# Kernel tuning notes

Hardware: AMD Instinct MI355X
Metric: run time of the kernel (lower is better)

Reference implementation:

```python
import jax, jax.numpy as jnp
import numpy as np

N_NODES = 50000
N_EDGES = 1250000
VOCAB = 50000
EMBED = 64
HIDDEN = 64
NUM_REL = 3
N_CLASSES = 2
N_GRAPHS = 512


def setup_inputs() -> dict:
    key = jax.random.key(0)
    ks = jax.random.split(key, 12)
    x = jax.random.randint(ks[0], (N_NODES,), 0, VOCAB, dtype=jnp.int32)
    edge_index = jax.random.randint(ks[1], (2, N_EDGES), 0, N_NODES, dtype=jnp.int32)
    edge_type = jax.random.randint(ks[2], (N_EDGES,), 0, NUM_REL, dtype=jnp.int32)
    batch = jnp.sort(jax.random.randint(ks[3], (N_NODES,), 0, N_GRAPHS, dtype=jnp.int32))
    s = 0.05
    emb = jax.random.normal(ks[4], (VOCAB, EMBED), jnp.float32) * s
    w1_rel = jax.random.normal(ks[5], (NUM_REL, EMBED, HIDDEN), jnp.float32) * s
    w1_root = jax.random.normal(ks[6], (EMBED, HIDDEN), jnp.float32) * s
    b1 = jnp.zeros((HIDDEN,), jnp.float32)
    w2_rel = jax.random.normal(ks[7], (NUM_REL, HIDDEN, HIDDEN), jnp.float32) * s
    w2_root = jax.random.normal(ks[8], (HIDDEN, HIDDEN), jnp.float32) * s
    b2 = jnp.zeros((HIDDEN,), jnp.float32)
    lin_w = jax.random.normal(ks[9], (HIDDEN, N_CLASSES), jnp.float32) * s
    lin_b = jnp.zeros((N_CLASSES,), jnp.float32)
    return {"x": x, "edge_index": edge_index, "edge_type": edge_type, "batch": batch,
            "emb": emb, "w1_rel": w1_rel, "w1_root": w1_root, "b1": b1,
            "w2_rel": w2_rel, "w2_root": w2_root, "b2": b2,
            "lin_w": lin_w, "lin_b": lin_b}


def rgcn_conv(h, src, dst, edge_type, w_rel, w_root, bias):
    # PyG RGCNConv: out = h @ W_root + bias + sum_r mean-aggregated (h_src @ W_r)
    out = h @ w_root + bias
    h_src = h[src]  # [E, F] gather
    for r in range(NUM_REL):
        mask = (edge_type == r).astype(h.dtype)  # [E]
        m = (h_src @ w_rel[r]) * mask[:, None]   # [E, H]
        s = jax.ops.segment_sum(m, dst, num_segments=N_NODES)
        cnt = jax.ops.segment_sum(mask, dst, num_segments=N_NODES)
        out = out + s / jnp.maximum(cnt, 1.0)[:, None]
    return out


def reference(x, edge_index, edge_type, batch, emb, w1_rel, w1_root, b1,
              w2_rel, w2_root, b2, lin_w, lin_b):
    src, dst = edge_index[0], edge_index[1]
    emb_eff = emb.at[0].set(0.0)  # padding_idx=0
    h = emb_eff[x]  # [N, EMBED]
    h = jax.nn.relu(rgcn_conv(h, src, dst, edge_type, w1_rel, w1_root, b1))
    h = jax.nn.relu(rgcn_conv(h, src, dst, edge_type, w2_rel, w2_root, b2))
    # global mean pool over graphs
    sums = jax.ops.segment_sum(h, batch, num_segments=N_GRAPHS)
    cnt = jax.ops.segment_sum(jnp.ones((h.shape[0],), h.dtype), batch, num_segments=N_GRAPHS)
    pooled = sums / jnp.maximum(cnt, 1.0)[:, None]  # [G, HIDDEN]
    return pooled @ lin_w + lin_b  # [G, N_CLASSES]
```

## Files before the change

### kernel.cpp

```cpp
#include <hip/hip_runtime.h>

#define CHUNK 2048

__global__ __launch_bounds__(256) void embed_count_kernel(
    const int* __restrict__ x, const float* __restrict__ emb, float* __restrict__ h0,
    const int* __restrict__ ei, int* __restrict__ pcount,
    int n_nodes, int n_edges, int n_bkt, int embed_blocks)
{
    __shared__ int cnt[512];
    int t = threadIdx.x;
    if ((int)blockIdx.x < embed_blocks) {
        int tt = blockIdx.x * 256 + t;
        if (tt < n_nodes * 16) {
            int n = tt >> 4, q = tt & 15;
            int xv = x[n];
            float4 v = {0.f, 0.f, 0.f, 0.f};
            if (xv != 0) v = *(const float4*)(emb + (size_t)xv * 64 + q * 4);
            *(float4*)(h0 + (size_t)n * 64 + q * 4) = v;
        }
        return;
    }
    int jb = blockIdx.x - embed_blocks;
    for (int b = t; b < 512; b += 256) cnt[b] = 0;
    __syncthreads();
    int base = jb * CHUNK;
#pragma unroll
    for (int i = 0; i < CHUNK / 256; ++i) {
        int e = base + i * 256 + t;
        if (e < n_edges) atomicAdd(&cnt[ei[n_edges + e] >> 7], 1);
    }
    __syncthreads();
    for (int b = t; b < n_bkt; b += 256) pcount[jb * n_bkt + b] = cnt[b];
}

__global__ __launch_bounds__(256) void colscan_kernel(
    const int* __restrict__ pcount, int* __restrict__ pre,
    int* __restrict__ totals, int* __restrict__ rowstartR,
    int n_chk, int n_bkt, int n_edges, int n_nodes)
{
    __shared__ int ps[256];
    int b = blockIdx.x, t = threadIdx.x;
    if (b == 0 && t == 0) rowstartR[4 * n_nodes] = n_edges;
    int v[4], s = 0;
#pragma unroll
    for (int i = 0; i < 4; ++i) {
        int jj = t * 4 + i;
        v[i] = (jj < n_chk) ? pcount[jj * n_bkt + b] : 0;
        s += v[i];
    }
    ps[t] = s;
    __syncthreads();
    for (int o = 1; o < 256; o <<= 1) {
        int u = (t >= o) ? ps[t - o] : 0;
        __syncthreads();
        ps[t] += u;
        __syncthreads();
    }
    int run = (t > 0) ? ps[t - 1] : 0;
#pragma unroll
    for (int i = 0; i < 4; ++i) {
        int jj = t * 4 + i;
        if (jj < n_chk) pre[jj * n_bkt + b] = run;
        run += v[i];
    }
    if (t == 255) totals[b] = run;
}

__global__ __launch_bounds__(256) void scatter_kernel(
    const int* __restrict__ ei, const int* __restrict__ et,
    const int* __restrict__ pre, const int* __restrict__ totals,
    int* __restrict__ esort, int* __restrict__ bucket_start,
    int n_edges, int n_bkt)
{
    __shared__ int bs[512], fill2[512], ps[256];
    int t = threadIdx.x, j = blockIdx.x;
    int a0 = (2 * t < n_bkt) ? totals[2 * t] : 0;
    int a1 = (2 * t + 1 < n_bkt) ? totals[2 * t + 1] : 0;
    ps[t] = a0 + a1;
    __syncthreads();
    for (int o = 1; o < 256; o <<= 1) {
        int u = (t >= o) ? ps[t - o] : 0;
        __syncthreads();
        ps[t] += u;
        __syncthreads();
    }
    int basex = (t > 0) ? ps[t - 1] : 0;
    bs[2 * t] = basex;
    bs[2 * t + 1] = basex + a0;
    fill2[t] = 0; fill2[t + 256] = 0;
    __syncthreads();
    if (j == 0) {
        for (int b = t; b < n_bkt; b += 256) bucket_start[b] = bs[b];
        if (t == 0) bucket_start[n_bkt] = n_edges;
    }
    for (int b = t; b < n_bkt; b += 256) bs[b] += pre[j * n_bkt + b];
    __syncthreads();
    int base = j * CHUNK;
#pragma unroll
    for (int i = 0; i < CHUNK / 256; ++i) {
        int e = base + i * 256 + t;
        if (e < n_edges) {
            int s = ei[e], d = ei[n_edges + e], r = et[e];
            int b = d >> 7;
            int pos = bs[b] + atomicAdd(&fill2[b], 1);
            esort[pos] = s | (r << 16) | ((d & 127) << 18);
        }
    }
}

__global__ __launch_bounds__(256) void bucket_sort_kernel(
    const int* __restrict__ bucket_start, int* __restrict__ esort,
    int* __restrict__ scratch, int* __restrict__ rowstartR, int n_nodes)
{
    __shared__ int cnt[512], off[512], fill[512], ps[256];
    int t = threadIdx.x, b = blockIdx.x;
    int s = bucket_start[b], e = bucket_start[b + 1];
    cnt[t] = 0; cnt[t + 256] = 0; fill[t] = 0; fill[t + 256] = 0;
    __syncthreads();
    int* scr = scratch + (size_t)b * 8192;
    for (int i = s + t; i < e; i += 256) {
        int p = esort[i];
        scr[i - s] = p;
        atomicAdd(&cnt[(p >> 16) & 0x1FF], 1);
    }
    __syncthreads();
    int a0 = cnt[2 * t], a1 = cnt[2 * t + 1];
    ps[t] = a0 + a1;
    __syncthreads();
    for (int o = 1; o < 256; o <<= 1) {
        int v = (t >= o) ? ps[t - o] : 0;
        __syncthreads();
        ps[t] += v;
        __syncthreads();
    }
    int basex = (t > 0) ? ps[t - 1] : 0;
    off[2 * t] = basex;
    off[2 * t + 1] = basex + a0;
    __syncthreads();
    int d0 = b * 128 + (2 * t >> 2);
    if (d0 < n_nodes) rowstartR[b * 512 + 2 * t] = s + off[2 * t];
    int d1 = b * 128 + ((2 * t + 1) >> 2);
    if (d1 < n_nodes) rowstartR[b * 512 + 2 * t + 1] = s + off[2 * t + 1];
    __syncthreads();
    for (int i = s + t; i < e; i += 256) {
        int p = scr[i - s];
        int bin = (p >> 16) & 0x1FF;
        int pos = s + off[bin] + atomicAdd(&fill[bin], 1);
        esort[pos] = p;
    }
}

__global__ __launch_bounds__(256) void agg_kernel(
    const float* __restrict__ hin, const int* __restrict__ rowstartR,
    const int* __restrict__ esort, float* __restrict__ means, int n_nodes)
{
    int wid = (blockIdx.x * 256 + threadIdx.x) >> 6;
    int lane = threadIdx.x & 63;
    if (wid >= n_nodes) return;
    int q = lane >> 4;
    int c = lane & 15;
    int4 rs = *(const int4*)(rowstartR + wid * 4);
    int s = rs.x, e = rs.w;

    float4 a0 = {0.f,0.f,0.f,0.f}, a1 = {0.f,0.f,0.f,0.f}, a2 = {0.f,0.f,0.f,0.f};

    int i = s + 4 * q;
    for (; i + 4 <= e; i += 16) {
        int p0 = esort[i], p1 = esort[i + 1], p2 = esort[i + 2], p3 = esort[i + 3];
        float4 v0 = *(const float4*)(hin + (size_t)(p0 & 0xFFFF) * 64 + c * 4);
        float4 v1 = *(const float4*)(hin + (size_t)(p1 & 0xFFFF) * 64 + c * 4);
        float4 v2 = *(const float4*)(hin + (size_t)(p2 & 0xFFFF) * 64 + c * 4);
        float4 v3 = *(const float4*)(hin + (size_t)(p3 & 0xFFFF) * 64 + c * 4);
#pragma unroll
        for (int m = 0; m < 4; ++m) {
            int p = m == 0 ? p0 : m == 1 ? p1 : m == 2 ? p2 : p3;
            float4 v = m == 0 ? v0 : m == 1 ? v1 : m == 2 ? v2 : v3;
            int r = (p >> 16) & 3;
            float m0 = (r == 0) ? 1.f : 0.f;
            float m1 = (r == 1) ? 1.f : 0.f;
            float m2 = (r == 2) ? 1.f : 0.f;
            a0.x = fmaf(m0, v.x, a0.x); a0.y = fmaf(m0, v.y, a0.y);
            a0.z = fmaf(m0, v.z, a0.z); a0.w = fmaf(m0, v.w, a0.w);
            a1.x = fmaf(m1, v.x, a1.x); a1.y = fmaf(m1, v.y, a1.y);
            a1.z = fmaf(m1, v.z, a1.z); a1.w = fmaf(m1, v.w, a1.w);
            a2.x = fmaf(m2, v.x, a2.x); a2.y = fmaf(m2, v.y, a2.y);
            a2.z = fmaf(m2, v.z, a2.z); a2.w = fmaf(m2, v.w, a2.w);
        }
    }
#pragma unroll
    for (int m = 0; m < 3; ++m) {
        int ii = i + m;
        if (ii < e) {
            int p = esort[ii];
            float4 v = *(const float4*)(hin + (size_t)(p & 0xFFFF) * 64 + c * 4);
            int r = (p >> 16) & 3;
            float m0 = (r == 0) ? 1.f : 0.f;
            float m1 = (r == 1) ? 1.f : 0.f;
            float m2 = (r == 2) ? 1.f : 0.f;
            a0.x = fmaf(m0, v.x, a0.x); a0.y = fmaf(m0, v.y, a0.y);
            a0.z = fmaf(m0, v.z, a0.z); a0.w = fmaf(m0, v.w, a0.w);
            a1.x = fmaf(m1, v.x, a1.x); a1.y = fmaf(m1, v.y, a1.y);
            a1.z = fmaf(m1, v.z, a1.z); a1.w = fmaf(m1, v.w, a1.w);
            a2.x = fmaf(m2, v.x, a2.x); a2.y = fmaf(m2, v.y, a2.y);
            a2.z = fmaf(m2, v.z, a2.z); a2.w = fmaf(m2, v.w, a2.w);
        }
    }
#pragma unroll
    for (int off = 16; off < 64; off <<= 1) {
        a0.x += __shfl_xor(a0.x, off); a0.y += __shfl_xor(a0.y, off);
        a0.z += __shfl_xor(a0.z, off); a0.w += __shfl_xor(a0.w, off);
        a1.x += __shfl_xor(a1.x, off); a1.y += __shfl_xor(a1.y, off);
        a1.z += __shfl_xor(a1.z, off); a1.w += __shfl_xor(a1.w, off);
        a2.x += __shfl_xor(a2.x, off); a2.y += __shfl_xor(a2.y, off);
        a2.z += __shfl_xor(a2.z, off); a2.w += __shfl_xor(a2.w, off);
    }
    if (q < 3) {
        int cnt = (q == 0) ? (rs.y - rs.x) : (q == 1) ? (rs.z - rs.y) : (rs.w - rs.z);
        float4 a = (q == 0) ? a0 : (q == 1) ? a1 : a2;
        float inv = 1.f / (float)max(cnt, 1);
        float4 m = {a.x * inv, a.y * inv, a.z * inv, a.w * inv};
        *(float4*)(means + (size_t)wid * 192 + q * 64 + c * 4) = m;
    }
}

__global__ __launch_bounds__(256) void transform_kernel(
    const float* __restrict__ hin, const float* __restrict__ means,
    const float* __restrict__ wroot, const float* __restrict__ wrel,
    const float* __restrict__ bias, float* __restrict__ hout, int n_nodes)
{
    __shared__ float wsh[2][4096];
    int t = threadIdx.x;
    int gt = blockIdx.x * 256 + t;
    int g = gt >> 4, q = gt & 15;
    int n0 = g * 4;
    bool active = (n0 < n_nodes);

    {
        const float4* sp = (const float4*)wroot;
        float4* d = (float4*)wsh[0];
#pragma unroll
        for (int i = 0; i < 4; ++i) d[t + i * 256] = sp[t + i * 256];
    }

    float4 acc[4];
    float4 b = {0.f, 0.f, 0.f, 0.f};
    if (active) b = *(const float4*)(bias + q * 4);
#pragma unroll
    for (int i = 0; i < 4; ++i) acc[i] = b;

    const float* hv = hin + (size_t)n0 * 64;
    const float* mv = means + (size_t)n0 * 192;

    for (int s = 0; s < 4; ++s) {
        __syncthreads();
        if (s < 3) {
            const float4* sp = (const float4*)wrel + (size_t)s * 1024;
            float4* d = (float4*)wsh[(s + 1) & 1];
#pragma unroll
            for (int i = 0; i < 4; ++i) d[t + i * 256] = sp[t + i * 256];
        }
        const float* vbase = (s == 0) ? hv : (mv + (s - 1) * 64);
        int vstride = (s == 0) ? 64 : 192;
        const float* wbuf = wsh[s & 1];
        if (active) {
#pragma unroll 4
            for (int k4 = 0; k4 < 16; ++k4) {
                float4 v[4];
#pragma unroll
                for (int i = 0; i < 4; ++i)
                    v[i] = *(const float4*)(vbase + i * vstride + k4 * 4);
#pragma unroll
                for (int kk = 0; kk < 4; ++kk) {
                    float4 w = *(const float4*)(wbuf + (k4 * 4 + kk) * 64 + q * 4);
#pragma unroll
                    for (int i = 0; i < 4; ++i) {
                        float sv = kk == 0 ? v[i].x : kk == 1 ? v[i].y : kk == 2 ? v[i].z : v[i].w;
                        acc[i].x = fmaf(sv, w.x, acc[i].x);
                        acc[i].y = fmaf(sv, w.y, acc[i].y);
                        acc[i].z = fmaf(sv, w.z, acc[i].z);
                        acc[i].w = fmaf(sv, w.w, acc[i].w);
                    }
                }
            }
        }
    }
    if (active) {
        float* o = hout + (size_t)n0 * 64 + q * 4;
#pragma unroll
        for (int i = 0; i < 4; ++i) {
            float4 r = {fmaxf(acc[i].x, 0.f), fmaxf(acc[i].y, 0.f),
                        fmaxf(acc[i].z, 0.f), fmaxf(acc[i].w, 0.f)};
            *(float4*)(o + i * 64) = r;
        }
    }
}

__global__ __launch_bounds__(256) void pool_kernel(
    const float* __restrict__ h2, const int* __restrict__ batch,
    const float* __restrict__ linw, const float* __restrict__ linb,
    float* __restrict__ out, int n_nodes, int n_graphs)
{
    int wid = (blockIdx.x * 256 + threadIdx.x) >> 6;
    int lane = threadIdx.x & 63;
    if (wid >= n_graphs) return;
    int g = wid;
    int lo = 0, hi = n_nodes;
    while (lo < hi) { int mid = (lo + hi) >> 1; if (batch[mid] < g) lo = mid + 1; else hi = mid; }
    int s = lo;
    lo = 0; hi = n_nodes;
    while (lo < hi) { int mid = (lo + hi) >> 1; if (batch[mid] < g + 1) lo = mid + 1; else hi = mid; }
    int e = lo;
    float sum = 0.f;
    for (int n = s; n < e; ++n) sum += h2[(size_t)n * 64 + lane];
    float mean = sum / (float)max(e - s, 1);
    float d0 = mean * linw[lane * 2 + 0];
    float d1 = mean * linw[lane * 2 + 1];
    for (int off = 32; off > 0; off >>= 1) {
        d0 += __shfl_down(d0, off);
        d1 += __shfl_down(d1, off);
    }
    if (lane == 0) {
        out[g * 2 + 0] = d0 + linb[0];
        out[g * 2 + 1] = d1 + linb[1];
    }
}

extern "C" void kernel_launch(void* const* d_in, const int* in_sizes, int n_in,
                              void* d_out, int out_size, void* d_ws, size_t ws_size,
                              hipStream_t stream)
{
    const int*   x      = (const int*)d_in[0];
    const int*   ei     = (const int*)d_in[1];
    const int*   et     = (const int*)d_in[2];
    const int*   batch  = (const int*)d_in[3];
    const float* emb    = (const float*)d_in[4];
    const float* w1rel  = (const float*)d_in[5];
    const float* w1root = (const float*)d_in[6];
    const float* b1     = (const float*)d_in[7];
    const float* w2rel  = (const float*)d_in[8];
    const float* w2root = (const float*)d_in[9];
    const float* b2     = (const float*)d_in[10];
    const float* linw   = (const float*)d_in[11];
    const float* linb   = (const float*)d_in[12];
    float* out = (float*)d_out;

    const int N = in_sizes[0];
    const int E = in_sizes[2];
    const int G = out_size / 2;
    const int NBKT = (N + 127) >> 7;
    const int NCHK = (E + CHUNK - 1) / CHUNK;

    float* hA        = (float*)d_ws;
    float* hB        = hA + (size_t)N * 64;
    float* means     = hB + (size_t)N * 64;
    int*   esort     = (int*)(means + (size_t)N * 192);
    int*   rowstartR = esort + E;
    int*   bucket_start = rowstartR + 4 * N + 4;
    int*   totals    = bucket_start + NBKT + 1;
    int*   scratch   = (int*)means;
    int*   pcount    = (int*)means + 4 * 1024 * 1024;
    int*   pre       = (int*)means + 5 * 1024 * 1024;

    int embedBlocks = (N * 16 + 255) / 256;
    embed_count_kernel<<<embedBlocks + NCHK, 256, 0, stream>>>(
        x, emb, hA, ei, pcount, N, E, NBKT, embedBlocks);
    colscan_kernel<<<NBKT, 256, 0, stream>>>(pcount, pre, totals, rowstartR, NCHK, NBKT, E, N);
    scatter_kernel<<<NCHK, 256, 0, stream>>>(ei, et, pre, totals, esort, bucket_start, E, NBKT);
    bucket_sort_kernel<<<NBKT, 256, 0, stream>>>(bucket_start, esort, scratch, rowstartR, N);

    int aggBlocks = (N * 64 + 255) / 256;
    int tfBlocks  = ((N + 3) / 4 * 16 + 255) / 256;
    agg_kernel<<<aggBlocks, 256, 0, stream>>>(hA, rowstartR, esort, means, N);
    transform_kernel<<<tfBlocks, 256, 0, stream>>>(hA, means, w1root, w1rel, b1, hB, N);
    agg_kernel<<<aggBlocks, 256, 0, stream>>>(hB, rowstartR, esort, means, N);
    transform_kernel<<<tfBlocks, 256, 0, stream>>>(hB, means, w2root, w2rel, b2, hA, N);

    pool_kernel<<<(G * 64 + 255) / 256, 256, 0, stream>>>(hA, batch, linw, linb, out, N, G);
}
```

Baseline: 339.1 us.

## Fuse mean-pool and linear head into second transform via per-node atomics

Removes the separate pool kernel. Each node's ReLU output is projected onto the two classifier columns, scaled by a precomputed inverse graph size, and accumulated into the output with atomics, all inside the layer-2 transform. The graph-size inverses and the bias initialisation are computed in extra blocks added to the colscan kernel. This also avoids writing the final hidden state to memory, at the cost of 2 atomics per node and non-deterministic float summation order.

```diff
diff --git a/kernel.cpp b/kernel.cpp
--- a/kernel.cpp
+++ b/kernel.cpp
@@ -36,10 +36,26 @@
 __global__ __launch_bounds__(256) void colscan_kernel(
     const int* __restrict__ pcount, int* __restrict__ pre,
     int* __restrict__ totals, int* __restrict__ rowstartR,
-    int n_chk, int n_bkt, int n_edges, int n_nodes)
+    const int* __restrict__ batch, const float* __restrict__ linb,
+    float* __restrict__ inv_cnt, float* __restrict__ outg,
+    int n_chk, int n_bkt, int n_edges, int n_nodes, int n_graphs)
 {
     __shared__ int ps[256];
     int b = blockIdx.x, t = threadIdx.x;
+    if (b >= n_bkt) {
+        int g = (b - n_bkt) * 256 + t;
+        if (g < n_graphs) {
+            int lo = 0, hi = n_nodes;
+            while (lo < hi) { int mid = (lo + hi) >> 1; if (batch[mid] < g) lo = mid + 1; else hi = mid; }
+            int s = lo;
+            lo = 0; hi = n_nodes;
+            while (lo < hi) { int mid = (lo + hi) >> 1; if (batch[mid] < g + 1) lo = mid + 1; else hi = mid; }
+            inv_cnt[g] = 1.f / (float)max(lo - s, 1);
+            outg[2 * g + 0] = linb[0];
+            outg[2 * g + 1] = linb[1];
+        }
+        return;
+    }
     if (b == 0 && t == 0) rowstartR[4 * n_nodes] = n_edges;
     int v[4], s = 0;
 #pragma unroll
@@ -226,7 +242,10 @@
 __global__ __launch_bounds__(256) void transform_kernel(
     const float* __restrict__ hin, const float* __restrict__ means,
     const float* __restrict__ wroot, const float* __restrict__ wrel,
-    const float* __restrict__ bias, float* __restrict__ hout, int n_nodes)
+    const float* __restrict__ bias, float* __restrict__ hout,
+    const int* __restrict__ batch, const float* __restrict__ linw,
+    const float* __restrict__ inv_cnt, float* __restrict__ outg,
+    int n_nodes, int do_pool)
 {
     __shared__ float wsh[2][4096];
     int t = threadIdx.x;
@@ -284,44 +303,47 @@
             }
         }
     }
-    if (active) {
-        float* o = hout + (size_t)n0 * 64 + q * 4;
+    if (!do_pool) {
+        if (active) {
+            float* o = hout + (size_t)n0 * 64 + q * 4;
+#pragma unroll
+            for (int i = 0; i < 4; ++i) {
+                float4 r = {fmaxf(acc[i].x, 0.f), fmaxf(acc[i].y, 0.f),
+                            fmaxf(acc[i].z, 0.f), fmaxf(acc[i].w, 0.f)};
+                *(float4*)(o + i * 64) = r;
+            }
+        }
+    } else if (active) {
+        float4 lwA = *(const float4*)(linw + q * 8);
+        float4 lwB = *(const float4*)(linw + q * 8 + 4);
+        float d0[4], d1[4];
 #pragma unroll
         for (int i = 0; i < 4; ++i) {
             float4 r = {fmaxf(acc[i].x, 0.f), fmaxf(acc[i].y, 0.f),
                         fmaxf(acc[i].z, 0.f), fmaxf(acc[i].w, 0.f)};
-            *(float4*)(o + i * 64) = r;
-        }
-    }
-}
-
-__global__ __launch_bounds__(256) void pool_kernel(
-    const float* __restrict__ h2, const int* __restrict__ batch,
-    const float* __restrict__ linw, const float* __restrict__ linb,
-    float* __restrict__ out, int n_nodes, int n_graphs)
-{
-    int wid = (blockIdx.x * 256 + threadIdx.x) >> 6;
-    int lane = threadIdx.x & 63;
-    if (wid >= n_graphs) return;
-    int g = wid;
-    int lo = 0, hi = n_nodes;
-    while (lo < hi) { int mid = (lo + hi) >> 1; if (batch[mid] < g) lo = mid + 1; else hi = mid; }
-    int s = lo;
-    lo = 0; hi = n_nodes;
-    while (lo < hi) { int mid = (lo + hi) >> 1; if (batch[mid] < g + 1) lo = mid + 1; else hi = mid; }
-    int e = lo;
-    float sum = 0.f;
-    for (int n = s; n < e; ++n) sum += h2[(size_t)n * 64 + lane];
-    float mean = sum / (float)max(e - s, 1);
-    float d0 = mean * linw[lane * 2 + 0];
-    float d1 = mean * linw[lane * 2 + 1];
-    for (int off = 32; off > 0; off >>= 1) {
-        d0 += __shfl_down(d0, off);
-        d1 += __shfl_down(d1, off);
-    }
-    if (lane == 0) {
-        out[g * 2 + 0] = d0 + linb[0];
-        out[g * 2 + 1] = d1 + linb[1];
+            d0[i] = r.x * lwA.x + r.y * lwA.z + r.z * lwB.x + r.w * lwB.z;
+            d1[i] = r.x * lwA.y + r.y * lwA.w + r.z * lwB.y + r.w * lwB.w;
+        }
+#pragma unroll
+        for (int off = 1; off < 16; off <<= 1) {
+#pragma unroll
+            for (int i = 0; i < 4; ++i) {
+                d0[i] += __shfl_xor(d0[i], off);
+                d1[i] += __shfl_xor(d1[i], off);
+            }
+        }
+        if (q == 0) {
+#pragma unroll
+            for (int i = 0; i < 4; ++i) {
+                int n = n0 + i;
+                if (n < n_nodes) {
+                    int gg = batch[n];
+                    float ic = inv_cnt[gg];
+                    atomicAdd(&outg[2 * gg + 0], d0[i] * ic);
+                    atomicAdd(&outg[2 * gg + 1], d1[i] * ic);
+                }
+            }
+        }
     }
 }
 
@@ -357,6 +379,7 @@
     int*   rowstartR = esort + E;
     int*   bucket_start = rowstartR + 4 * N + 4;
     int*   totals    = bucket_start + NBKT + 1;
+    float* inv_cnt   = (float*)(totals + NBKT);
     int*   scratch   = (int*)means;
     int*   pcount    = (int*)means + 4 * 1024 * 1024;
     int*   pre       = (int*)means + 5 * 1024 * 1024;
@@ -364,16 +387,19 @@
     int embedBlocks = (N * 16 + 255) / 256;
     embed_count_kernel<<<embedBlocks + NCHK, 256, 0, stream>>>(
         x, emb, hA, ei, pcount, N, E, NBKT, embedBlocks);
-    colscan_kernel<<<NBKT, 256, 0, stream>>>(pcount, pre, totals, rowstartR, NCHK, NBKT, E, N);
+    int gBlocks = (G + 255) / 256;
+    colscan_kernel<<<NBKT + gBlocks, 256, 0, stream>>>(
+        pcount, pre, totals, rowstartR, batch, linb, inv_cnt, out,
+        NCHK, NBKT, E, N, G);
     scatter_kernel<<<NCHK, 256, 0, stream>>>(ei, et, pre, totals, esort, bucket_start, E, NBKT);
     bucket_sort_kernel<<<NBKT, 256, 0, stream>>>(bucket_start, esort, scratch, rowstartR, N);
 
     int aggBlocks = (N * 64 + 255) / 256;
     int tfBlocks  = ((N + 3) / 4 * 16 + 255) / 256;
     agg_kernel<<<aggBlocks, 256, 0, stream>>>(hA, rowstartR, esort, means, N);
-    transform_kernel<<<tfBlocks, 256, 0, stream>>>(hA, means, w1root, w1rel, b1, hB, N);
+    transform_kernel<<<tfBlocks, 256, 0, stream>>>(
+        hA, means, w1root, w1rel, b1, hB, batch, linw, inv_cnt, out, N, 0);
     agg_kernel<<<aggBlocks, 256, 0, stream>>>(hB, rowstartR, esort, means, N);
-    transform_kernel<<<tfBlocks, 256, 0, stream>>>(hB, means, w2root, w2rel, b2, hA, N);
-
-    pool_kernel<<<(G * 64 + 255) / 256, 256, 0, stream>>>(hA, batch, linw, linb, out, N, G);
-}
+    transform_kernel<<<tfBlocks, 256, 0, stream>>>(
+        hB, means, w2root, w2rel, b2, hA, batch, linw, inv_cnt, out, N, 1);
+}
```

Result: slower. 367.8 us (+8.5%).
